# Kernel tuning notes

Hardware: AMD Instinct MI355X
Metric: run time of the kernel (lower is better)

## Reference

```python
import math
import jax, jax.numpy as jnp
import numpy as np


def _cirlen(scale):
    # replicates UpSample.get_cirlen: smallest rational period of the scale
    for i in (10, 100, 1000, 10000):
        y = scale * i
        x = i
        if y == math.floor(y):
            break
    y = int(round(y))
    g = math.gcd(x, y)
    return y // g


def _proj(out_len, scale, scale_int, in_len):
    # replicates matmask_made: for each output coord, source coord and repeat index (sca),
    # giving the selected column p = coord*scale_int + sca in the nearest-repeated grid.
    c = np.arange(out_len, dtype=np.float64)
    c[-1] -= 0.1
    coord = np.floor(c / scale).astype(np.int64)
    sca = np.arange(out_len) - np.searchsorted(coord, coord)  # occurrence index per coord
    p = coord * scale_int + sca
    # unfold(kernel=3, dilation=2, padding=2): taps at p-2, p, p+2 in the upscaled grid
    q = p[:, None] + 2 * np.array([-1, 0, 1], dtype=np.int64)[None, :]
    valid = ((q >= 0) & (q < in_len * scale_int)).astype(np.float32)
    src = np.clip(q // scale_int, 0, in_len - 1)  # upscaled pixel q == original pixel q//scale_int
    return src, valid


def reference(x, w1, b1, w2, b2, ln_g, ln_b, scale_x10):
    scale = round(scale_x10 / 10.0, 4)
    scale_int = math.ceil(scale)
    N, C, H, W = x.shape
    outH = math.ceil(scale * H)
    outW = math.ceil(scale * W)
    cycle = _cirlen(scale)
    K = 9 * C

    # ---- per-cycle-position dynamic weights (Scale2Pos_mat + Fea2Weight + LayerNorm) ----
    off = np.arange(cycle, dtype=np.float64) / scale
    off = (off - np.floor(off)).astype(np.float32)
    oh_i, ow_j = np.meshgrid(off, off, indexing='ij')  # row index = i*cycle + j
    posmat = np.stack([np.full_like(oh_i, 1.0 / scale), oh_i, ow_j], axis=-1).reshape(-1, 3)
    posmat = jnp.asarray(posmat)
    h = jax.nn.relu(posmat @ w1 + b1)                       # (cyc^2, 256)
    wflat = h @ w2 + b2                                     # (cyc^2, 9*C*outC)
    outC = wflat.shape[-1] // K
    wv = wflat.reshape(cycle * cycle, outC, K)              # view(pos, outC, K)
    mu = wv.mean(-1, keepdims=True)
    var = wv.var(-1, keepdims=True)                         # biased, as torch LayerNorm
    wv = ((wv - mu) / jnp.sqrt(var + 1e-5)) * ln_g + ln_b
    wv = wv / C
    Wm = jnp.transpose(wv, (0, 2, 1)).reshape(cycle, cycle, K, outC)

    # ---- irregular gather (nearest-repeat + unfold + mask_select), done as direct gather ----
    rs, vh = _proj(outH, scale, scale_int, H)  # (outH,3)
    cs, vw = _proj(outW, scale, scale_int, W)  # (outW,3)
    g = x[:, :, jnp.asarray(rs), :]            # (N,C,outH,3,W)
    g = g[:, :, :, :, jnp.asarray(cs)]         # (N,C,outH,3,outW,3)
    g = g * jnp.asarray(vh)[None, None, :, :, None, None]
    g = g * jnp.asarray(vw)[None, None, None, None, :, :]
    # unfold channel order is (C, kh, kw)
    patch = jnp.transpose(g, (0, 2, 4, 1, 3, 5)).reshape(N, outH, outW, K)

    # ---- pad to cycle multiple, per-cycle-position matmul, crop ----
    Hp = -(-outH // cycle) * cycle
    Wp = -(-outW // cycle) * cycle
    patch = jnp.pad(patch, ((0, 0), (0, Hp - outH), (0, Wp - outW), (0, 0)))
    patch = patch.reshape(N, Hp // cycle, cycle, Wp // cycle, cycle, K)
    out = jnp.einsum('nhiwjk,ijkc->nchiwj', patch, Wm)
    out = out.reshape(N, outC, Hp, Wp)[:, :, :outH, :outW]
    return out


def setup_inputs() -> dict:
    key = jax.random.key(0)
    k = jax.random.split(key, 5)
    inC, outC = 64, 3
    x = jax.random.normal(k[0], (8, inC, 96, 96), dtype=jnp.float32)
    w1 = jax.random.normal(k[1], (3, 256), dtype=jnp.float32) * 0.5
    b1 = jax.random.normal(k[2], (256,), dtype=jnp.float32) * 0.1
    w2 = jax.random.normal(k[3], (256, 9 * inC * outC), dtype=jnp.float32) * 0.0625
    b2 = jax.random.normal(k[4], (9 * inC * outC,), dtype=jnp.float32) * 0.01
    ln_g = jnp.ones((9 * inC,), dtype=jnp.float32)
    ln_b = jnp.zeros((9 * inC,), dtype=jnp.float32)
    return {"x": x, "w1": w1, "b1": b1, "w2": w2, "b2": b2,
            "ln_g": ln_g, "ln_b": ln_b, "scale_x10": 15}
```

## Files before the change

### kernel.cpp

```cpp
#include <hip/hip_runtime.h>
#include <math.h>

#define C_IN   64
#define HW_IN  96
#define N_B    8
#define OUTC   3
#define OUT_HW 144
#define HID    256
#define KDIM   576
#define NFLAT  1728

#define WS_W    0
#define WS_RS   15552
#define WS_VH   15984
#define WS_WF   16416

__global__ __launch_bounds__(64) void a1_wflat(
    const float* __restrict__ w1, const float* __restrict__ b1,
    const float* __restrict__ w2, const float* __restrict__ b2,
    const int* __restrict__ sxp, float* __restrict__ ws)
{
    __shared__ float h[HID];
    const int cell = blockIdx.x;
    const int tile = blockIdx.y;
    const int lane = threadIdx.x;

    double scale = (double)sxp[0] / 10.0;
    int ci = cell / 3, cj = cell % 3;
    double oi = (double)ci / scale; oi -= floor(oi);
    double oj = (double)cj / scale; oj -= floor(oj);
    float p0 = (float)(1.0 / scale), p1 = (float)oi, p2 = (float)oj;

    #pragma unroll
    for (int q = 0; q < 4; ++q) {
        int p = lane + 64 * q;
        float hv = b1[p] + p0 * w1[p] + p1 * w1[HID + p] + p2 * w1[2 * HID + p];
        h[p] = fmaxf(hv, 0.f);
    }
    __syncthreads();

    const int col = tile * 64 + lane;
    float v = b2[col];
    const float* w2c = w2 + col;
    #pragma unroll 32
    for (int p = 0; p < HID; ++p) v += h[p] * w2c[(size_t)p * NFLAT];
    ws[WS_WF + cell * NFLAT + col] = v;
}

__global__ __launch_bounds__(256) void a2_ln_pack_proj(
    const float* __restrict__ ln_g, const float* __restrict__ ln_b,
    const int* __restrict__ sxp, float* __restrict__ ws)
{
    __shared__ float wf[NFLAT];
    __shared__ float rsum[4], rsum2[4];
    const int cell = blockIdx.x, tid = threadIdx.x;

    const float* wfg = ws + WS_WF + cell * NFLAT;
    for (int k = tid; k < NFLAT; k += 256) wf[k] = wfg[k];
    __syncthreads();

    const int lane = tid & 63, wid = tid >> 6;
    for (int co = 0; co < OUTC; ++co) {
        float s = 0.f, s2 = 0.f;
        for (int k = tid; k < KDIM; k += 256) { float v = wf[co * KDIM + k]; s += v; s2 += v * v; }
        #pragma unroll
        for (int off = 32; off > 0; off >>= 1) { s += __shfl_down(s, off); s2 += __shfl_down(s2, off); }
        __syncthreads();
        if (lane == 0) { rsum[wid] = s; rsum2[wid] = s2; }
        __syncthreads();
        float S  = rsum[0] + rsum[1] + rsum[2] + rsum[3];
        float Q  = rsum2[0] + rsum2[1] + rsum2[2] + rsum2[3];
        float mu = S * (1.f / KDIM);
        float rstd = rsqrtf(Q * (1.f / KDIM) - mu * mu + 1e-5f);
        for (int k = tid; k < KDIM; k += 256) {
            float v = ((wf[co * KDIM + k] - mu) * rstd * ln_g[k] + ln_b[k]) * (1.f / C_IN);
            int c = k / 9, t = k % 9;
            ws[WS_W + cell * NFLAT + c * 27 + t * 3 + co] = v;
        }
    }

    if (cell == 0 && tid < OUT_HW) {
        double scale = (double)sxp[0] / 10.0;
        int scale_int = (int)ceil(scale - 1e-9);
        double cc = (double)tid; if (tid == OUT_HW - 1) cc -= 0.1;
        long coord = (long)floor(cc / scale);
        long first = (long)ceil((double)coord * scale);
        long p = coord * (long)scale_int + ((long)tid - first);
        #pragma unroll
        for (int d = 0; d < 3; ++d) {
            long q = p + 2 * (d - 1);
            bool ok = (q >= 0) && (q < (long)HW_IN * scale_int);
            long src = (q < 0) ? 0 : q / scale_int;
            if (src > HW_IN - 1) src = HW_IN - 1;
            ws[WS_RS + tid * 3 + d] = (float)src;
            ws[WS_VH + tid * 3 + d] = ok ? 1.f : 0.f;
        }
    }
}

#define JSTRIDE 2056

__global__ __launch_bounds__(192) void c_main(
    const float* __restrict__ x, const float* __restrict__ ws,
    float* __restrict__ out)
{
    __shared__ float Wl[3 * JSTRIDE];
    const int tid = threadIdx.x;
    const int oh  = blockIdx.x;
    const int n   = blockIdx.y;
    const int i   = oh % 3;

    for (int idx = tid; idx < 3 * 64 * 32; idx += 192) {
        int j = idx >> 11;
        int rem = idx & 2047;
        int c = rem >> 5, m = rem & 31;
        float v = 0.f;
        if (m < 27) v = ws[WS_W + (size_t)((i * 3 + j) * 64 + c) * 27 + m];
        Wl[j * JSTRIDE + c * 32 + m] = v;
    }
    __syncthreads();

    const int ow = tid;
    if (ow >= OUT_HW) return;

    const float* rsf = ws + WS_RS;
    const float* vhf = ws + WS_VH;
    const int jj = ow % 3;
    const float* Wj = Wl + jj * JSTRIDE;

    int s[3]; float vw[3];
    #pragma unroll
    for (int d = 0; d < 3; ++d) { s[d] = (int)rsf[ow * 3 + d]; vw[d] = vhf[ow * 3 + d]; }

    int xoff[9]; float vv[9];
    #pragma unroll
    for (int dr = 0; dr < 3; ++dr) {
        int r = (int)rsf[oh * 3 + dr];
        float vhd = vhf[oh * 3 + dr];
        #pragma unroll
        for (int dc = 0; dc < 3; ++dc) {
            xoff[dr * 3 + dc] = r * HW_IN + s[dc];
            vv[dr * 3 + dc]   = vhd * vw[dc];
        }
    }

    const float* xb = x + (size_t)n * C_IN * HW_IN * HW_IN;
    float acc[3] = {0.f, 0.f, 0.f};

    #pragma unroll 2
    for (int c = 0; c < C_IN; ++c) {
        const float* xc = xb + c * (HW_IN * HW_IN);
        float w[28];
        const float4* wp = (const float4*)(Wj + c * 32);
        #pragma unroll
        for (int q = 0; q < 7; ++q) ((float4*)w)[q] = wp[q];
        #pragma unroll
        for (int t = 0; t < 9; ++t) {
            float xv = xc[xoff[t]] * vv[t];
            acc[0] += xv * w[t * 3 + 0];
            acc[1] += xv * w[t * 3 + 1];
            acc[2] += xv * w[t * 3 + 2];
        }
    }

    #pragma unroll
    for (int co = 0; co < OUTC; ++co)
        out[((size_t)(n * OUTC + co) * OUT_HW + oh) * OUT_HW + ow] = acc[co];
}

extern "C" void kernel_launch(void* const* d_in, const int* in_sizes, int n_in,
                              void* d_out, int out_size, void* d_ws, size_t ws_size,
                              hipStream_t stream)
{
    const float* x    = (const float*)d_in[0];
    const float* w1   = (const float*)d_in[1];
    const float* b1   = (const float*)d_in[2];
    const float* w2   = (const float*)d_in[3];
    const float* b2   = (const float*)d_in[4];
    const float* ln_g = (const float*)d_in[5];
    const float* ln_b = (const float*)d_in[6];
    const int*   sx   = (const int*)d_in[7];
    float* ws  = (float*)d_ws;
    float* out = (float*)d_out;

    a1_wflat<<<dim3(9, 27), 64, 0, stream>>>(w1, b1, w2, b2, sx, ws);
    a2_ln_pack_proj<<<9, 256, 0, stream>>>(ln_g, ln_b, sx, ws);
    c_main<<<dim3(OUT_HW, N_B), 192, 0, stream>>>(x, ws, out);
}
```

Before: 127.5 us.

## Split weight-gen reduction across waves and process two batch images per main block

The weight-generation kernel now splits the 256-long hidden reduction across four waves with a shared-memory partial sum, giving each block more parallelism. The LayerNorm kernel is parallelized over output channels in a second grid dimension and reads directly from global memory instead of staging the whole row in LDS. The main kernel has each block compute two batch images (n and n+4), amortizing the per-block LDS weight staging over twice the work while halving the grid. The trade-off is more registers and fewer blocks in the main kernel.

```diff
diff --git a/kernel.cpp b/kernel.cpp
--- a/kernel.cpp
+++ b/kernel.cpp
@@ -15,15 +15,16 @@
 #define WS_VH   15984
 #define WS_WF   16416
 
-__global__ __launch_bounds__(64) void a1_wflat(
+__global__ __launch_bounds__(256) void a1_wflat(
     const float* __restrict__ w1, const float* __restrict__ b1,
     const float* __restrict__ w2, const float* __restrict__ b2,
     const int* __restrict__ sxp, float* __restrict__ ws)
 {
     __shared__ float h[HID];
+    __shared__ float part[4 * 64];
     const int cell = blockIdx.x;
     const int tile = blockIdx.y;
-    const int lane = threadIdx.x;
+    const int tid  = threadIdx.x;
 
     double scale = (double)sxp[0] / 10.0;
     int ci = cell / 3, cj = cell % 3;
@@ -31,55 +32,55 @@
     double oj = (double)cj / scale; oj -= floor(oj);
     float p0 = (float)(1.0 / scale), p1 = (float)oi, p2 = (float)oj;
 
-    #pragma unroll
-    for (int q = 0; q < 4; ++q) {
-        int p = lane + 64 * q;
-        float hv = b1[p] + p0 * w1[p] + p1 * w1[HID + p] + p2 * w1[2 * HID + p];
-        h[p] = fmaxf(hv, 0.f);
-    }
-    __syncthreads();
-
-    const int col = tile * 64 + lane;
-    float v = b2[col];
-    const float* w2c = w2 + col;
-    #pragma unroll 32
-    for (int p = 0; p < HID; ++p) v += h[p] * w2c[(size_t)p * NFLAT];
-    ws[WS_WF + cell * NFLAT + col] = v;
+    float hv = b1[tid] + p0 * w1[tid] + p1 * w1[HID + tid] + p2 * w1[2 * HID + tid];
+    h[tid] = fmaxf(hv, 0.f);
+    __syncthreads();
+
+    const int wave = tid >> 6, lane = tid & 63;
+    const int col  = tile * 64 + lane;
+    const float* w2c = w2 + (size_t)(wave * 64) * NFLAT + col;
+    const float* hp  = h + wave * 64;
+    float v = 0.f;
+    #pragma unroll
+    for (int r = 0; r < 64; ++r) v += hp[r] * w2c[(size_t)r * NFLAT];
+    part[wave * 64 + lane] = v;
+    __syncthreads();
+
+    if (tid < 64) {
+        int c2 = tile * 64 + tid;
+        float s = b2[c2] + part[tid] + part[64 + tid] + part[128 + tid] + part[192 + tid];
+        ws[WS_WF + cell * NFLAT + c2] = s;
+    }
 }
 
 __global__ __launch_bounds__(256) void a2_ln_pack_proj(
     const float* __restrict__ ln_g, const float* __restrict__ ln_b,
     const int* __restrict__ sxp, float* __restrict__ ws)
 {
-    __shared__ float wf[NFLAT];
     __shared__ float rsum[4], rsum2[4];
-    const int cell = blockIdx.x, tid = threadIdx.x;
-
-    const float* wfg = ws + WS_WF + cell * NFLAT;
-    for (int k = tid; k < NFLAT; k += 256) wf[k] = wfg[k];
-    __syncthreads();
-
+    const int cell = blockIdx.x, co = blockIdx.y, tid = threadIdx.x;
     const int lane = tid & 63, wid = tid >> 6;
-    for (int co = 0; co < OUTC; ++co) {
-        float s = 0.f, s2 = 0.f;
-        for (int k = tid; k < KDIM; k += 256) { float v = wf[co * KDIM + k]; s += v; s2 += v * v; }
-        #pragma unroll
-        for (int off = 32; off > 0; off >>= 1) { s += __shfl_down(s, off); s2 += __shfl_down(s2, off); }
-        __syncthreads();
-        if (lane == 0) { rsum[wid] = s; rsum2[wid] = s2; }
-        __syncthreads();
-        float S  = rsum[0] + rsum[1] + rsum[2] + rsum[3];
-        float Q  = rsum2[0] + rsum2[1] + rsum2[2] + rsum2[3];
-        float mu = S * (1.f / KDIM);
-        float rstd = rsqrtf(Q * (1.f / KDIM) - mu * mu + 1e-5f);
-        for (int k = tid; k < KDIM; k += 256) {
-            float v = ((wf[co * KDIM + k] - mu) * rstd * ln_g[k] + ln_b[k]) * (1.f / C_IN);
-            int c = k / 9, t = k % 9;
-            ws[WS_W + cell * NFLAT + c * 27 + t * 3 + co] = v;
-        }
-    }
-
-    if (cell == 0 && tid < OUT_HW) {
+
+    const float* wfc = ws + WS_WF + cell * NFLAT + co * KDIM;
+
+    float s = 0.f, s2 = 0.f;
+    for (int k = tid; k < KDIM; k += 256) { float v = wfc[k]; s += v; s2 += v * v; }
+    #pragma unroll
+    for (int off = 32; off > 0; off >>= 1) { s += __shfl_down(s, off); s2 += __shfl_down(s2, off); }
+    if (lane == 0) { rsum[wid] = s; rsum2[wid] = s2; }
+    __syncthreads();
+    float S  = rsum[0] + rsum[1] + rsum[2] + rsum[3];
+    float Q  = rsum2[0] + rsum2[1] + rsum2[2] + rsum2[3];
+    float mu = S * (1.f / KDIM);
+    float rstd = rsqrtf(Q * (1.f / KDIM) - mu * mu + 1e-5f);
+
+    for (int k = tid; k < KDIM; k += 256) {
+        float v = ((wfc[k] - mu) * rstd * ln_g[k] + ln_b[k]) * (1.f / C_IN);
+        int c = k / 9, t = k % 9;
+        ws[WS_W + cell * NFLAT + c * 27 + t * 3 + co] = v;
+    }
+
+    if (cell == 0 && co == 0 && tid < OUT_HW) {
         double scale = (double)sxp[0] / 10.0;
         int scale_int = (int)ceil(scale - 1e-9);
         double cc = (double)tid; if (tid == OUT_HW - 1) cc -= 0.1;
@@ -107,7 +108,7 @@
     __shared__ float Wl[3 * JSTRIDE];
     const int tid = threadIdx.x;
     const int oh  = blockIdx.x;
-    const int n   = blockIdx.y;
+    const int n0  = blockIdx.y;
     const int i   = oh % 3;
 
     for (int idx = tid; idx < 3 * 64 * 32; idx += 192) {
@@ -144,28 +145,38 @@
         }
     }
 
-    const float* xb = x + (size_t)n * C_IN * HW_IN * HW_IN;
-    float acc[3] = {0.f, 0.f, 0.f};
+    const float* xb0 = x + (size_t)n0 * C_IN * HW_IN * HW_IN;
+    const float* xb1 = xb0 + (size_t)4 * C_IN * HW_IN * HW_IN;
+    float acc[2][3] = {{0.f,0.f,0.f},{0.f,0.f,0.f}};
 
     #pragma unroll 2
     for (int c = 0; c < C_IN; ++c) {
-        const float* xc = xb + c * (HW_IN * HW_IN);
+        const float* xc0 = xb0 + c * (HW_IN * HW_IN);
+        const float* xc1 = xb1 + c * (HW_IN * HW_IN);
         float w[28];
         const float4* wp = (const float4*)(Wj + c * 32);
         #pragma unroll
         for (int q = 0; q < 7; ++q) ((float4*)w)[q] = wp[q];
         #pragma unroll
         for (int t = 0; t < 9; ++t) {
-            float xv = xc[xoff[t]] * vv[t];
-            acc[0] += xv * w[t * 3 + 0];
-            acc[1] += xv * w[t * 3 + 1];
-            acc[2] += xv * w[t * 3 + 2];
+            float xv0 = xc0[xoff[t]] * vv[t];
+            float xv1 = xc1[xoff[t]] * vv[t];
+            acc[0][0] += xv0 * w[t * 3 + 0];
+            acc[0][1] += xv0 * w[t * 3 + 1];
+            acc[0][2] += xv0 * w[t * 3 + 2];
+            acc[1][0] += xv1 * w[t * 3 + 0];
+            acc[1][1] += xv1 * w[t * 3 + 1];
+            acc[1][2] += xv1 * w[t * 3 + 2];
         }
     }
 
     #pragma unroll
-    for (int co = 0; co < OUTC; ++co)
-        out[((size_t)(n * OUTC + co) * OUT_HW + oh) * OUT_HW + ow] = acc[co];
+    for (int rr = 0; rr < 2; ++rr) {
+        int n = n0 + rr * 4;
+        #pragma unroll
+        for (int co = 0; co < OUTC; ++co)
+            out[((size_t)(n * OUTC + co) * OUT_HW + oh) * OUT_HW + ow] = acc[rr][co];
+    }
 }
 
 extern "C" void kernel_launch(void* const* d_in, const int* in_sizes, int n_in,
@@ -183,7 +194,7 @@
     float* ws  = (float*)d_ws;
     float* out = (float*)d_out;
 
-    a1_wflat<<<dim3(9, 27), 64, 0, stream>>>(w1, b1, w2, b2, sx, ws);
-    a2_ln_pack_proj<<<9, 256, 0, stream>>>(ln_g, ln_b, sx, ws);
-    c_main<<<dim3(OUT_HW, N_B), 192, 0, stream>>>(x, ws, out);
-}
+    a1_wflat<<<dim3(9, 27), 256, 0, stream>>>(w1, b1, w2, b2, sx, ws);
+    a2_ln_pack_proj<<<dim3(9, 3), 256, 0, stream>>>(ln_g, ln_b, sx, ws);
+    c_main<<<dim3(OUT_HW, 4), 192, 0, stream>>>(x, ws, out);
+}
```

Result: slower. 137.8 us (+8.1%).
